# Optimization experiments

Hardware: AMD Instinct MI355X
Metric: run time of the kernel (lower is better)

Reference implementation:

```python
import jax, jax.numpy as jnp
import numpy as np

DIM = 192
WINDOW = 8
HEADS = 6
N = WINDOW * WINDOW


def _relative_position_index(ws):
    coords = np.stack(np.meshgrid(np.arange(ws), np.arange(ws), indexing='ij'))  # (2, ws, ws)
    flat = coords.reshape(2, -1)  # (2, N)
    rel = flat[:, :, None] - flat[:, None, :]  # (2, N, N)
    rel = rel.transpose(1, 2, 0).copy()
    rel[:, :, 0] += ws - 1
    rel[:, :, 1] += ws - 1
    rel[:, :, 0] *= 2 * ws - 1
    return rel.sum(-1).astype(np.int32)  # (N, N)


def setup_inputs() -> dict:
    key = jax.random.key(0)
    ks = jax.random.split(key, 5)
    B_ = 4096
    x = jax.random.normal(ks[0], (B_, N, DIM), dtype=jnp.float32)
    qkv_w = jax.random.normal(ks[1], (3 * DIM, DIM), dtype=jnp.float32) * 0.02
    qkv_b = jnp.zeros((3 * DIM,), dtype=jnp.float32)
    proj_w = jax.random.normal(ks[2], (DIM, DIM), dtype=jnp.float32) * 0.02
    proj_b = jnp.zeros((DIM,), dtype=jnp.float32)
    rpb_table = jax.random.normal(ks[3], ((2 * WINDOW - 1) ** 2, HEADS), dtype=jnp.float32) * 0.02
    rel_idx = jnp.asarray(_relative_position_index(WINDOW))
    return {"x": x, "qkv_w": qkv_w, "qkv_b": qkv_b, "proj_w": proj_w,
            "proj_b": proj_b, "rpb_table": rpb_table, "rel_idx": rel_idx}


def reference(x, qkv_w, qkv_b, proj_w, proj_b, rpb_table, rel_idx):
    B_, n, C = x.shape
    d = C // HEADS
    scale = d ** -0.5
    qkv = x @ qkv_w.T + qkv_b                      # (B_, N, 3C)
    qkv = qkv.reshape(B_, n, 3, HEADS, d).transpose(2, 0, 3, 1, 4)  # (3, B_, H, N, d)
    q, k, v = qkv[0], qkv[1], qkv[2]
    attn = jnp.einsum('bhnd,bhmd->bhnm', q * scale, k)  # (B_, H, N, N)
    bias = rpb_table[rel_idx.reshape(-1)].reshape(n, n, HEADS).transpose(2, 0, 1)  # (H, N, N)
    attn = jax.nn.softmax(attn + bias[None], axis=-1)
    out = jnp.einsum('bhnm,bhmd->bnhd', attn, v).reshape(B_, n, C)
    return out @ proj_w.T + proj_b
```

## Files before the change

### kernel.cpp

```cpp
#include <hip/hip_runtime.h>


constexpr int NT = 64, DIMC = 192, NH = 6;
constexpr float SC = 0.17677669529663687f;

typedef short          s8v __attribute__((ext_vector_type(8)));
typedef float          f4v __attribute__((ext_vector_type(4)));
typedef unsigned short u4v __attribute__((ext_vector_type(4)));

constexpr size_t WS_QKVW  = 0;
constexpr size_t WS_PROJW = WS_QKVW + (size_t)36*6*2*1024;
constexpr size_t WS_BIAS  = WS_PROJW + (size_t)12*6*2*1024;
constexpr size_t WS_QKVB  = WS_BIAS + (size_t)6*4*4*64*16;
constexpr size_t WS_NEED  = WS_QKVB + (size_t)576*4;

__device__ __forceinline__ unsigned short bhi(float x) {
  return (unsigned short)(__builtin_bit_cast(unsigned int, x) >> 16);
}
__device__ __forceinline__ float bft(unsigned short h) {
  return __builtin_bit_cast(float, ((unsigned int)h) << 16);
}
__device__ __forceinline__ unsigned short brne(float x) {
  unsigned int u = __builtin_bit_cast(unsigned int, x);
  u += 0x7FFFu + ((u >> 16) & 1u);
  return (unsigned short)(u >> 16);
}

#define MFMA16(a, b, c) __builtin_amdgcn_mfma_f32_16x16x32_bf16((a), (b), (c), 0, 0, 0)

__device__ __forceinline__ s8v ld_frag(const unsigned short* base, int idx) {
  u4v a = *(const u4v*)(base + idx);
  u4v b = *(const u4v*)(base + idx + 16);
  s8v r;
  #pragma unroll
  for (int i = 0; i < 4; ++i) { r[i] = (short)a[i]; r[4 + i] = (short)b[i]; }
  return r;
}

__global__ __launch_bounds__(256) void prep_kernel(
    const float* __restrict__ qkv_w, const float* __restrict__ qkv_b,
    const float* __restrict__ proj_w, const float* __restrict__ rpb,
    const int* __restrict__ ridx, char* __restrict__ ws)
{
  const int t = blockIdx.x * 256 + threadIdx.x;
  if (t < 13824) {
    const int lane = t & 63, rest = t >> 6;
    const int kk = rest % 6, nt = rest / 6;
    const int g = lane >> 4, c = lane & 15;
    const int n = 16 * nt + c;
    const float sc = (nt < 12) ? SC : 1.f;
    const float* p = qkv_w + n * 192 + kk * 32 + 4 * g;
    f4v a = *(const f4v*)p;       a *= sc;
    f4v b = *(const f4v*)(p + 16); b *= sc;
    s8v hi, lo;
    #pragma unroll
    for (int i = 0; i < 4; ++i) {
      unsigned short h0 = bhi(a[i]); hi[i]     = (short)h0; lo[i]     = (short)brne(a[i] - bft(h0));
      unsigned short h1 = bhi(b[i]); hi[4 + i] = (short)h1; lo[4 + i] = (short)brne(b[i] - bft(h1));
    }
    s8v* base = (s8v*)(ws + WS_QKVW);
    base[((nt * 6 + kk) * 2 + 0) * 64 + lane] = hi;
    base[((nt * 6 + kk) * 2 + 1) * 64 + lane] = lo;
  } else if (t < 18432) {
    const int t2 = t - 13824;
    const int lane = t2 & 63, rest = t2 >> 6;
    const int h = rest % 6, nt = rest / 6;
    const int g = lane >> 4, c = lane & 15;
    const int n = 16 * nt + c;
    const float* p = proj_w + n * 192 + 32 * h + 4 * g;
    f4v a = *(const f4v*)p;
    f4v b = *(const f4v*)(p + 16);
    s8v hi, lo;
    #pragma unroll
    for (int i = 0; i < 4; ++i) {
      unsigned short h0 = bhi(a[i]); hi[i]     = (short)h0; lo[i]     = (short)brne(a[i] - bft(h0));
      unsigned short h1 = bhi(b[i]); hi[4 + i] = (short)h1; lo[4 + i] = (short)brne(b[i] - bft(h1));
    }
    s8v* base = (s8v*)(ws + WS_PROJW);
    base[((nt * 6 + h) * 2 + 0) * 64 + lane] = hi;
    base[((nt * 6 + h) * 2 + 1) * 64 + lane] = lo;
  } else if (t < 24576) {
    const int t2 = t - 18432;
    const int lane = t2 & 63, rest = t2 >> 6;
    const int nt = rest & 3, mt = (rest >> 2) & 3, h = rest >> 4;
    const int g = lane >> 4, c = lane & 15;
    const int q = 16 * nt + c;
    const int kb = 16 * mt + 4 * g;
    const int* ip = ridx + q * 64 + kb;
    f4v o;
    #pragma unroll
    for (int r = 0; r < 4; ++r) o[r] = rpb[ip[r] * 6 + h];
    ((f4v*)(ws + WS_BIAS))[((h * 4 + mt) * 4 + nt) * 64 + lane] = o;
  } else if (t < 25152) {
    const int i = t - 24576;
    ((float*)(ws + WS_QKVB))[i] = qkv_b[i] * (i < 192 ? SC : 1.f);
  }
}


__device__ __forceinline__ void qkv_head(int lane, const float* __restrict__ xbase,
                                         const s8v* __restrict__ qkvw,
                                         int h, f4v acc[6]) {
  #pragma unroll
  for (int j = 0; j < 6; ++j)
    #pragma unroll
    for (int r = 0; r < 4; ++r) acc[j][r] = 0.f;
  #pragma unroll
  for (int kk = 0; kk < 6; ++kk) {
    f4v xa = *(const f4v*)(xbase + 32 * kk);
    f4v xb = *(const f4v*)(xbase + 32 * kk + 16);
    s8v ah, al;
    #pragma unroll
    for (int i = 0; i < 4; ++i) {
      unsigned short h0 = bhi(xa[i]); ah[i]     = (short)h0; al[i]     = (short)brne(xa[i] - bft(h0));
      unsigned short h1 = bhi(xb[i]); ah[4 + i] = (short)h1; al[4 + i] = (short)brne(xb[i] - bft(h1));
    }
    #pragma unroll
    for (int sgj = 0; sgj < 6; ++sgj) {
      const int seg = sgj >> 1, j = sgj & 1;
      const int n576 = seg * 12 + 2 * h + j;
      const s8v bh = qkvw[((n576 * 6 + kk) * 2 + 0) * 64 + lane];
      const s8v bl = qkvw[((n576 * 6 + kk) * 2 + 1) * 64 + lane];
      acc[sgj] = MFMA16(ah, bh, acc[sgj]);
      acc[sgj] = MFMA16(ah, bl, acc[sgj]);
      acc[sgj] = MFMA16(al, bh, acc[sgj]);
    }
  }
}

__device__ __forceinline__ void qkv_stage(int wv, int g, int c,
    const f4v acc[6], const float* __restrict__ qkvb, int h,
    unsigned short* Qh_, unsigned short* Ql_,
    unsigned short* Kh_, unsigned short* Kl_,
    unsigned short* Vh_, unsigned short* Vl_) {
  #pragma unroll
  for (int sgj = 0; sgj < 6; ++sgj) {
    const int seg = sgj >> 1, j = sgj & 1;
    const float bv = qkvb[seg * 192 + 32 * h + 16 * j + c];
    if (seg < 2) {
      unsigned short* dh = (seg == 0) ? Qh_ : Kh_;
      unsigned short* dl = (seg == 0) ? Ql_ : Kl_;
      #pragma unroll
      for (int r = 0; r < 4; ++r) {
        const float v = acc[sgj][r] + bv;
        const unsigned short hh = bhi(v);
        dh[(16 * wv + 4 * g + r) * 36 + 16 * j + c] = hh;
        dl[(16 * wv + 4 * g + r) * 36 + 16 * j + c] = brne(v - bft(hh));
      }
    } else {
      u4v hh, ll;
      #pragma unroll
      for (int r = 0; r < 4; ++r) {
        const float v = acc[sgj][r] + bv;
        const unsigned short x0 = bhi(v);
        hh[r] = x0; ll[r] = brne(v - bft(x0));
      }
      *(u4v*)&Vh_[(16 * j + c) * 68 + 16 * wv + 4 * g] = hh;
      *(u4v*)&Vl_[(16 * j + c) * 68 + 16 * wv + 4 * g] = ll;
    }
  }
}

__device__ __forceinline__ void proj_acc(int lane, const s8v oh, const s8v ol,
                                         const s8v* __restrict__ projw, int h,
                                         f4v pacc[12]) {
  #pragma unroll
  for (int nt = 0; nt < 12; ++nt) {
    const s8v wh = projw[((nt * 6 + h) * 2 + 0) * 64 + lane];
    const s8v wl = projw[((nt * 6 + h) * 2 + 1) * 64 + lane];
    pacc[nt] = MFMA16(oh, wh, pacc[nt]);
    pacc[nt] = MFMA16(oh, wl, pacc[nt]);
    pacc[nt] = MFMA16(ol, wh, pacc[nt]);
  }
}

template<bool DO_NEXT>
__device__ __forceinline__ void head_iter(
    int h, int lane, int wv, int g, int c,
    const float* __restrict__ xbase,
    const s8v* __restrict__ qkvw, const f4v* __restrict__ biasf,
    const float* __restrict__ qkvb,
    const unsigned short* Qhc, const unsigned short* Qlc,
    const unsigned short* Khc, const unsigned short* Klc,
    const unsigned short* Vhc, const unsigned short* Vlc,
    unsigned short* Qhn, unsigned short* Qln,
    unsigned short* Khn, unsigned short* Kln,
    unsigned short* Vhn, unsigned short* Vln,
    s8v& oh, s8v& ol)
{
  f4v sacc[4];
  #pragma unroll
  for (int mt = 0; mt < 4; ++mt)
    sacc[mt] = biasf[((h * 4 + mt) * 4 + wv) * 64 + lane];
  s8v qbh, qbl;
  {
    const int idx = (16 * wv + c) * 36 + 4 * g;
    qbh = ld_frag(Qhc, idx);
    qbl = ld_frag(Qlc, idx);
  }
  #pragma unroll
  for (int mt = 0; mt < 4; ++mt) {
    const int idx = (16 * mt + c) * 36 + 4 * g;
    const s8v kh = ld_frag(Khc, idx);
    const s8v kl = ld_frag(Klc, idx);
    sacc[mt] = MFMA16(kh, qbh, sacc[mt]);
    sacc[mt] = MFMA16(kh, qbl, sacc[mt]);
    sacc[mt] = MFMA16(kl, qbh, sacc[mt]);
  }

  f4v acc2[6];
  if (DO_NEXT) qkv_head(lane, xbase, qkvw, h + 1, acc2);

  float mx = sacc[0][0];
  #pragma unroll
  for (int mt = 0; mt < 4; ++mt)
    #pragma unroll
    for (int r = 0; r < 4; ++r) mx = fmaxf(mx, sacc[mt][r]);
  mx = fmaxf(mx, __shfl_xor(mx, 16));
  mx = fmaxf(mx, __shfl_xor(mx, 32));
  float pv[4][4];
  float sum = 0.f;
  #pragma unroll
  for (int mt = 0; mt < 4; ++mt)
    #pragma unroll
    for (int r = 0; r < 4; ++r) { pv[mt][r] = __expf(sacc[mt][r] - mx); sum += pv[mt][r]; }

  f4v oa0, oa1;
  #pragma unroll
  for (int r = 0; r < 4; ++r) { oa0[r] = 0.f; oa1[r] = 0.f; }
  #pragma unroll
  for (int kk = 0; kk < 2; ++kk) {
    s8v pbh, pbl;
    #pragma unroll
    for (int i = 0; i < 4; ++i) {
      const float v0 = pv[2 * kk][i];
      const float v1 = pv[2 * kk + 1][i];
      const unsigned short h0 = bhi(v0), h1 = bhi(v1);
      pbh[i]     = (short)h0; pbl[i]     = (short)brne(v0 - bft(h0));
      pbh[4 + i] = (short)h1; pbl[4 + i] = (short)brne(v1 - bft(h1));
    }
    #pragma unroll
    for (int mo = 0; mo < 2; ++mo) {
      const int idx = (16 * mo + c) * 68 + 32 * kk + 4 * g;
      const s8v vh = ld_frag(Vhc, idx);
      const s8v vl = ld_frag(Vlc, idx);
      f4v& o = (mo == 0) ? oa0 : oa1;
      o = MFMA16(vh, pbh, o);
      o = MFMA16(vh, pbl, o);
      o = MFMA16(vl, pbh, o);
    }
  }
  sum += __shfl_xor(sum, 16);
  sum += __shfl_xor(sum, 32);
  const float inv = 1.f / sum;

  #pragma unroll
  for (int i = 0; i < 4; ++i) {
    const float v0 = oa0[i] * inv;
    const unsigned short h0 = bhi(v0);
    oh[i] = (short)h0; ol[i] = (short)brne(v0 - bft(h0));
    const float v1 = oa1[i] * inv;
    const unsigned short h1 = bhi(v1);
    oh[4 + i] = (short)h1; ol[4 + i] = (short)brne(v1 - bft(h1));
  }

  if (DO_NEXT) qkv_stage(wv, g, c, acc2, qkvb, h + 1, Qhn, Qln, Khn, Kln, Vhn, Vln);
}

__global__ __launch_bounds__(256, 2)
void win_attn_mfma(const float* __restrict__ x, const float* __restrict__ proj_b,
                   const char* __restrict__ ws, float* __restrict__ out)
{
  __shared__ alignas(16) unsigned short QhS[2][64 * 36], QlS[2][64 * 36];
  __shared__ alignas(16) unsigned short KhS[2][64 * 36], KlS[2][64 * 36];
  __shared__ alignas(16) unsigned short VhS[2][32 * 68], VlS[2][32 * 68];

  const int tid = threadIdx.x;
  const int wv = tid >> 6, lane = tid & 63, g = lane >> 4, c = lane & 15;
  const size_t win = blockIdx.x;
  const float* xw   = x   + win * (size_t)(NT * DIMC);
  float*       outw = out + win * (size_t)(NT * DIMC);

  const s8v*   qkvw  = (const s8v*)(ws + WS_QKVW);
  const s8v*   projw = (const s8v*)(ws + WS_PROJW);
  const f4v*   biasf = (const f4v*)(ws + WS_BIAS);
  const float* qkvb  = (const float*)(ws + WS_QKVB);

  f4v pacc[12];
  #pragma unroll
  for (int i = 0; i < 12; ++i)
    #pragma unroll
    for (int r = 0; r < 4; ++r) pacc[i][r] = 0.f;

  const float* xbase = xw + (size_t)(16 * wv + c) * DIMC + 4 * g;

  {
    f4v acc0[6];
    qkv_head(lane, xbase, qkvw, 0, acc0);
    qkv_stage(wv, g, c, acc0, qkvb, 0,
              QhS[0], QlS[0], KhS[0], KlS[0], VhS[0], VlS[0]);
  }
  __syncthreads();

  s8v oh{}, ol{};

  head_iter<true>(0, lane, wv, g, c, xbase, qkvw, biasf, qkvb,
                  QhS[0], QlS[0], KhS[0], KlS[0], VhS[0], VlS[0],
                  QhS[1], QlS[1], KhS[1], KlS[1], VhS[1], VlS[1],
                  oh, ol);
  __syncthreads();

  #pragma unroll 1
  for (int h = 1; h < NH - 1; ++h) {
    const int p = h & 1;
    proj_acc(lane, oh, ol, projw, h - 1, pacc);
    head_iter<true>(h, lane, wv, g, c, xbase, qkvw, biasf, qkvb,
                    QhS[p], QlS[p], KhS[p], KlS[p], VhS[p], VlS[p],
                    QhS[p ^ 1], QlS[p ^ 1], KhS[p ^ 1], KlS[p ^ 1],
                    VhS[p ^ 1], VlS[p ^ 1],
                    oh, ol);
    __syncthreads();
  }

  proj_acc(lane, oh, ol, projw, 4, pacc);
  head_iter<false>(5, lane, wv, g, c, xbase, qkvw, biasf, qkvb,
                   QhS[1], QlS[1], KhS[1], KlS[1], VhS[1], VlS[1],
                   QhS[0], QlS[0], KhS[0], KlS[0], VhS[0], VlS[0],
                   oh, ol);
  proj_acc(lane, oh, ol, projw, 5, pacc);

  #pragma unroll
  for (int nt = 0; nt < 12; ++nt) {
    const float pb = proj_b[16 * nt + c];
    #pragma unroll
    for (int r = 0; r < 4; ++r)
      outw[(size_t)(16 * wv + 4 * g + r) * DIMC + 16 * nt + c] = pacc[nt][r] + pb;
  }
}

__global__ __launch_bounds__(256, 2)
void win_attn_kernel(const float* __restrict__ x, const float* __restrict__ qkv_w,
                     const float* __restrict__ qkv_b, const float* __restrict__ proj_w,
                     const float* __restrict__ proj_b, const float* __restrict__ rpb,
                     const int* __restrict__ ridx, float* __restrict__ out)
{
  __shared__ float reg1[32 * 192];
  __shared__ float reg2[48 * 64];
  __shared__ float qs[64 * 36];
  __shared__ float ks[64 * 36];
  __shared__ float vs[64 * 36];

  const int tid = threadIdx.x;
  const int w = blockIdx.x;
  const float* xw = x + (size_t)w * (NT * DIMC);
  float* outw = out + (size_t)w * (NT * DIMC);

  const int cg = tid >> 4;
  const int tgA = tid & 15;
  const int tB = tid >> 2;
  const int jB = tid & 3;
  const int ogD = tid >> 4;
  const int tgD = tid & 15;

  int idxv[16];
  #pragma unroll
  for (int mm = 0; mm < 16; ++mm) idxv[mm] = ridx[tB * 64 + jB + 4 * mm] * NH;

  float oacc[4][12];
  #pragma unroll
  for (int tt = 0; tt < 4; ++tt)
    #pragma unroll
    for (int oo = 0; oo < 12; ++oo) oacc[tt][oo] = 0.f;

  for (int h = 0; h < NH; ++h) {
    float acc[6][4];
    #pragma unroll
    for (int cc = 0; cc < 6; ++cc)
      #pragma unroll
      for (int tt = 0; tt < 4; ++tt) acc[cc][tt] = 0.f;

    for (int i0 = 0; i0 < DIMC; i0 += 48) {
      __syncthreads();
      #pragma unroll
      for (int k = 0; k < 12; ++k) {
        int flat = k * 256 + tid;
        int t = flat & 63, ii = flat >> 6;
        reg2[ii * 64 + t] = xw[t * DIMC + i0 + ii];
      }
      #pragma unroll
      for (int k = 0; k < 18; ++k) {
        int flat = k * 256 + tid;
        int rr = flat % 96, ii = flat / 96;
        int seg = rr >> 5, lc = rr & 31;
        int grow = seg * 192 + h * 32 + lc;
        reg1[ii * 96 + rr] = qkv_w[grow * DIMC + i0 + ii];
      }
      __syncthreads();
      #pragma unroll 2
      for (int i = 0; i < 48; ++i) {
        float4 x4 = *(const float4*)(&reg2[i * 64 + 4 * tgA]);
        const float* wr = &reg1[i * 96 + 6 * cg];
        float2 w0 = *(const float2*)(wr + 0);
        float2 w1 = *(const float2*)(wr + 2);
        float2 w2 = *(const float2*)(wr + 4);
        float xa[4] = {x4.x, x4.y, x4.z, x4.w};
        float wa[6] = {w0.x, w0.y, w1.x, w1.y, w2.x, w2.y};
        #pragma unroll
        for (int cc = 0; cc < 6; ++cc)
          #pragma unroll
          for (int tt = 0; tt < 4; ++tt)
            acc[cc][tt] = fmaf(wa[cc], xa[tt], acc[cc][tt]);
      }
    }
    #pragma unroll
    for (int cc = 0; cc < 6; ++cc) {
      int cch = 6 * cg + cc;
      int seg = cch >> 5, lc = cch & 31;
      float bv = qkv_b[seg * 192 + h * 32 + lc];
      if (seg == 0) {
        #pragma unroll
        for (int tt = 0; tt < 4; ++tt)
          qs[(4 * tgA + tt) * 36 + lc] = (acc[cc][tt] + bv) * SC;
      } else if (seg == 1) {
        #pragma unroll
        for (int tt = 0; tt < 4; ++tt)
          ks[(4 * tgA + tt) * 36 + lc] = acc[cc][tt] + bv;
      } else {
        #pragma unroll
        for (int tt = 0; tt < 4; ++tt)
          vs[(4 * tgA + tt) * 36 + lc] = acc[cc][tt] + bv;
      }
    }
    __syncthreads();

    #pragma unroll
    for (int k = 0; k < 24; ++k) {
      int flat = k * 256 + tid;
      int o = flat % 192, ccc = flat / 192;
      reg1[ccc * 192 + o] = proj_w[o * DIMC + h * 32 + ccc];
    }

    float qr[32];
    {
      const float* qrow = &qs[tB * 36];
      #pragma unroll
      for (int d4 = 0; d4 < 8; ++d4) {
        float4 q4 = *(const float4*)(qrow + 4 * d4);
        qr[4*d4+0] = q4.x; qr[4*d4+1] = q4.y; qr[4*d4+2] = q4.z; qr[4*d4+3] = q4.w;
      }
    }
    float sv[16];
    #pragma unroll
    for (int mm = 0; mm < 16; ++mm) {
      const float* krow = &ks[(jB + 4 * mm) * 36];
      float a = rpb[idxv[mm] + h];
      #pragma unroll
      for (int d4 = 0; d4 < 8; ++d4) {
        float4 k4 = *(const float4*)(krow + 4 * d4);
        a = fmaf(qr[4*d4+0], k4.x, a);
        a = fmaf(qr[4*d4+1], k4.y, a);
        a = fmaf(qr[4*d4+2], k4.z, a);
        a = fmaf(qr[4*d4+3], k4.w, a);
      }
      sv[mm] = a;
    }
    float mx = sv[0];
    #pragma unroll
    for (int mm = 1; mm < 16; ++mm) mx = fmaxf(mx, sv[mm]);
    mx = fmaxf(mx, __shfl_xor(mx, 1));
    mx = fmaxf(mx, __shfl_xor(mx, 2));
    float sum = 0.f;
    #pragma unroll
    for (int mm = 0; mm < 16; ++mm) { sv[mm] = __expf(sv[mm] - mx); sum += sv[mm]; }
    sum += __shfl_xor(sum, 1);
    sum += __shfl_xor(sum, 2);
    const float inv = 1.f / sum;

    float part[32];
    #pragma unroll
    for (int dd = 0; dd < 32; ++dd) part[dd] = 0.f;
    #pragma unroll
    for (int mm = 0; mm < 16; ++mm) {
      float pvv = sv[mm] * inv;
      const float* vrow = &vs[(jB + 4 * mm) * 36];
      #pragma unroll
      for (int d4 = 0; d4 < 8; ++d4) {
        float4 v4 = *(const float4*)(vrow + 4 * d4);
        part[4*d4+0] = fmaf(pvv, v4.x, part[4*d4+0]);
        part[4*d4+1] = fmaf(pvv, v4.y, part[4*d4+1]);
        part[4*d4+2] = fmaf(pvv, v4.z, part[4*d4+2]);
        part[4*d4+3] = fmaf(pvv, v4.w, part[4*d4+3]);
      }
    }
    float p16[16];
    {
      const bool hi2 = (jB & 1);
      #pragma unroll
      for (int k2 = 0; k2 < 16; ++k2) {
        float lo_v = part[k2], hi_v = part[16 + k2];
        float sendv = hi2 ? lo_v : hi_v;
        float keepv = hi2 ? hi_v : lo_v;
        float got = __shfl_xor(sendv, 1);
        p16[k2] = keepv + got;
      }
    }
    float p8[8];
    {
      const bool hi2 = (jB & 2);
      #pragma unroll
      for (int k2 = 0; k2 < 8; ++k2) {
        float lo_v = p16[k2], hi_v = p16[8 + k2];
        float sendv = hi2 ? lo_v : hi_v;
        float keepv = hi2 ? hi_v : lo_v;
        float got = __shfl_xor(sendv, 2);
        p8[k2] = keepv + got;
      }
    }
    const int dd0 = (jB & 1) * 16 + (jB & 2) * 4;
    #pragma unroll
    for (int k2 = 0; k2 < 8; ++k2)
      reg2[(dd0 + k2) * 64 + tB] = p8[k2];

    __syncthreads();

    {
      const int o0 = 12 * ogD, t0 = 4 * tgD;
      #pragma unroll 2
      for (int cc2 = 0; cc2 < 32; ++cc2) {
        float4 a4 = *(const float4*)(&reg2[cc2 * 64 + t0]);
        const float* pr = &reg1[cc2 * 192 + o0];
        float4 b0 = *(const float4*)(pr + 0);
        float4 b1 = *(const float4*)(pr + 4);
        float4 b2 = *(const float4*)(pr + 8);
        float av[4]  = {a4.x, a4.y, a4.z, a4.w};
        float bw[12] = {b0.x, b0.y, b0.z, b0.w, b1.x, b1.y, b1.z, b1.w,
                        b2.x, b2.y, b2.z, b2.w};
        #pragma unroll
        for (int tt = 0; tt < 4; ++tt)
          #pragma unroll
          for (int oo = 0; oo < 12; ++oo)
            oacc[tt][oo] = fmaf(av[tt], bw[oo], oacc[tt][oo]);
      }
    }
  }

  {
    const int o0 = 12 * ogD, t0 = 4 * tgD;
    #pragma unroll
    for (int oo = 0; oo < 12; ++oo) {
      float pb = proj_b[o0 + oo];
      #pragma unroll
      for (int tt = 0; tt < 4; ++tt)
        outw[(size_t)(t0 + tt) * DIMC + o0 + oo] = oacc[tt][oo] + pb;
    }
  }
}

extern "C" void kernel_launch(void* const* d_in, const int* in_sizes, int n_in,
                              void* d_out, int out_size, void* d_ws, size_t ws_size,
                              hipStream_t stream) {
  const float* x      = (const float*)d_in[0];
  const float* qkv_w  = (const float*)d_in[1];
  const float* qkv_b  = (const float*)d_in[2];
  const float* proj_w = (const float*)d_in[3];
  const float* proj_b = (const float*)d_in[4];
  const float* rpb    = (const float*)d_in[5];
  const int*   ridx   = (const int*)d_in[6];
  float* out = (float*)d_out;
  const int B = in_sizes[0] / (NT * DIMC);

  if (d_ws != nullptr && ws_size >= WS_NEED) {
    hipLaunchKernelGGL(prep_kernel, dim3(99), dim3(256), 0, stream,
                       qkv_w, qkv_b, proj_w, rpb, ridx, (char*)d_ws);
    hipLaunchKernelGGL(win_attn_mfma, dim3(B), dim3(256), 0, stream,
                       x, proj_b, (const char*)d_ws, out);
  } else {
    hipLaunchKernelGGL(win_attn_kernel, dim3(B), dim3(256), 0, stream,
                       x, qkv_w, qkv_b, proj_w, proj_b, rpb, ridx, out);
  }
}
```

Before: 937.4 us.

## Warp-specialize window attention into QKV producer and attention consumer waves

The block grows from 4 to 6 waves. Two producer waves compute the QKV projection for the next head into a double-buffered LDS area, while four consumer waves run attention, softmax and the output projection for the current head. The two roles hand off through block barriers. The intent is to overlap the QKV GEMM with attention work that the old code ran serially within each wave. The cost is that producer waves recompute x fragments for all four row tiles, and the larger 384-thread block with launch bounds (384,3) changes register pressure and occupancy.

```diff
diff --git a/kernel.cpp b/kernel.cpp
--- a/kernel.cpp
+++ b/kernel.cpp
@@ -97,177 +97,87 @@
   }
 }
 
-
-__device__ __forceinline__ void qkv_head(int lane, const float* __restrict__ xbase,
-                                         const s8v* __restrict__ qkvw,
-                                         int h, f4v acc[6]) {
+__device__ __forceinline__ void produce_qkv(
+    int p, int lane, int g, int c, int hh,
+    const float* __restrict__ xw,
+    const s8v* __restrict__ qkvw, const float* __restrict__ qkvb,
+    unsigned short* Qh_, unsigned short* Ql_,
+    unsigned short* Kh_, unsigned short* Kl_,
+    unsigned short* Vh_, unsigned short* Vl_)
+{
+  f4v acc[3][4];
   #pragma unroll
-  for (int j = 0; j < 6; ++j)
-    #pragma unroll
-    for (int r = 0; r < 4; ++r) acc[j][r] = 0.f;
+  for (int s = 0; s < 3; ++s)
+    #pragma unroll
+    for (int mt = 0; mt < 4; ++mt)
+      #pragma unroll
+      for (int r = 0; r < 4; ++r) acc[s][mt][r] = 0.f;
+
   #pragma unroll
   for (int kk = 0; kk < 6; ++kk) {
-    f4v xa = *(const f4v*)(xbase + 32 * kk);
-    f4v xb = *(const f4v*)(xbase + 32 * kk + 16);
-    s8v ah, al;
-    #pragma unroll
-    for (int i = 0; i < 4; ++i) {
-      unsigned short h0 = bhi(xa[i]); ah[i]     = (short)h0; al[i]     = (short)brne(xa[i] - bft(h0));
-      unsigned short h1 = bhi(xb[i]); ah[4 + i] = (short)h1; al[4 + i] = (short)brne(xb[i] - bft(h1));
-    }
-    #pragma unroll
-    for (int sgj = 0; sgj < 6; ++sgj) {
-      const int seg = sgj >> 1, j = sgj & 1;
-      const int n576 = seg * 12 + 2 * h + j;
-      const s8v bh = qkvw[((n576 * 6 + kk) * 2 + 0) * 64 + lane];
-      const s8v bl = qkvw[((n576 * 6 + kk) * 2 + 1) * 64 + lane];
-      acc[sgj] = MFMA16(ah, bh, acc[sgj]);
-      acc[sgj] = MFMA16(ah, bl, acc[sgj]);
-      acc[sgj] = MFMA16(al, bh, acc[sgj]);
-    }
-  }
-}
-
-__device__ __forceinline__ void qkv_stage(int wv, int g, int c,
-    const f4v acc[6], const float* __restrict__ qkvb, int h,
-    unsigned short* Qh_, unsigned short* Ql_,
-    unsigned short* Kh_, unsigned short* Kl_,
-    unsigned short* Vh_, unsigned short* Vl_) {
+    s8v bh[3], bl[3];
+    #pragma unroll
+    for (int s = 0; s < 3; ++s) {
+      const int sgj = 3 * p + s;
+      const int n576 = (sgj >> 1) * 12 + 2 * hh + (sgj & 1);
+      bh[s] = qkvw[((n576 * 6 + kk) * 2 + 0) * 64 + lane];
+      bl[s] = qkvw[((n576 * 6 + kk) * 2 + 1) * 64 + lane];
+    }
+    #pragma unroll
+    for (int mt = 0; mt < 4; ++mt) {
+      const float* xp = xw + (size_t)(16 * mt + c) * DIMC + 32 * kk + 4 * g;
+      f4v xa = *(const f4v*)xp;
+      f4v xb = *(const f4v*)(xp + 16);
+      s8v ah, al;
+      #pragma unroll
+      for (int i = 0; i < 4; ++i) {
+        unsigned short h0 = bhi(xa[i]); ah[i]     = (short)h0; al[i]     = (short)brne(xa[i] - bft(h0));
+        unsigned short h1 = bhi(xb[i]); ah[4 + i] = (short)h1; al[4 + i] = (short)brne(xb[i] - bft(h1));
+      }
+      #pragma unroll
+      for (int s = 0; s < 3; ++s) {
+        acc[s][mt] = MFMA16(ah, bh[s], acc[s][mt]);
+        acc[s][mt] = MFMA16(ah, bl[s], acc[s][mt]);
+        acc[s][mt] = MFMA16(al, bh[s], acc[s][mt]);
+      }
+    }
+  }
+
   #pragma unroll
-  for (int sgj = 0; sgj < 6; ++sgj) {
+  for (int s = 0; s < 3; ++s) {
+    const int sgj = 3 * p + s;
     const int seg = sgj >> 1, j = sgj & 1;
-    const float bv = qkvb[seg * 192 + 32 * h + 16 * j + c];
+    const float bv = qkvb[seg * 192 + 32 * hh + 16 * j + c];
     if (seg < 2) {
       unsigned short* dh = (seg == 0) ? Qh_ : Kh_;
       unsigned short* dl = (seg == 0) ? Ql_ : Kl_;
       #pragma unroll
-      for (int r = 0; r < 4; ++r) {
-        const float v = acc[sgj][r] + bv;
-        const unsigned short hh = bhi(v);
-        dh[(16 * wv + 4 * g + r) * 36 + 16 * j + c] = hh;
-        dl[(16 * wv + 4 * g + r) * 36 + 16 * j + c] = brne(v - bft(hh));
-      }
+      for (int mt = 0; mt < 4; ++mt)
+        #pragma unroll
+        for (int r = 0; r < 4; ++r) {
+          const float v = acc[s][mt][r] + bv;
+          const unsigned short hh0 = bhi(v);
+          dh[(16 * mt + 4 * g + r) * 36 + 16 * j + c] = hh0;
+          dl[(16 * mt + 4 * g + r) * 36 + 16 * j + c] = brne(v - bft(hh0));
+        }
     } else {
-      u4v hh, ll;
-      #pragma unroll
-      for (int r = 0; r < 4; ++r) {
-        const float v = acc[sgj][r] + bv;
-        const unsigned short x0 = bhi(v);
-        hh[r] = x0; ll[r] = brne(v - bft(x0));
-      }
-      *(u4v*)&Vh_[(16 * j + c) * 68 + 16 * wv + 4 * g] = hh;
-      *(u4v*)&Vl_[(16 * j + c) * 68 + 16 * wv + 4 * g] = ll;
-    }
-  }
-}
-
-__device__ __forceinline__ void proj_acc(int lane, const s8v oh, const s8v ol,
-                                         const s8v* __restrict__ projw, int h,
-                                         f4v pacc[12]) {
-  #pragma unroll
-  for (int nt = 0; nt < 12; ++nt) {
-    const s8v wh = projw[((nt * 6 + h) * 2 + 0) * 64 + lane];
-    const s8v wl = projw[((nt * 6 + h) * 2 + 1) * 64 + lane];
-    pacc[nt] = MFMA16(oh, wh, pacc[nt]);
-    pacc[nt] = MFMA16(oh, wl, pacc[nt]);
-    pacc[nt] = MFMA16(ol, wh, pacc[nt]);
-  }
-}
-
-template<bool DO_NEXT>
-__device__ __forceinline__ void head_iter(
-    int h, int lane, int wv, int g, int c,
-    const float* __restrict__ xbase,
-    const s8v* __restrict__ qkvw, const f4v* __restrict__ biasf,
-    const float* __restrict__ qkvb,
-    const unsigned short* Qhc, const unsigned short* Qlc,
-    const unsigned short* Khc, const unsigned short* Klc,
-    const unsigned short* Vhc, const unsigned short* Vlc,
-    unsigned short* Qhn, unsigned short* Qln,
-    unsigned short* Khn, unsigned short* Kln,
-    unsigned short* Vhn, unsigned short* Vln,
-    s8v& oh, s8v& ol)
-{
-  f4v sacc[4];
-  #pragma unroll
-  for (int mt = 0; mt < 4; ++mt)
-    sacc[mt] = biasf[((h * 4 + mt) * 4 + wv) * 64 + lane];
-  s8v qbh, qbl;
-  {
-    const int idx = (16 * wv + c) * 36 + 4 * g;
-    qbh = ld_frag(Qhc, idx);
-    qbl = ld_frag(Qlc, idx);
-  }
-  #pragma unroll
-  for (int mt = 0; mt < 4; ++mt) {
-    const int idx = (16 * mt + c) * 36 + 4 * g;
-    const s8v kh = ld_frag(Khc, idx);
-    const s8v kl = ld_frag(Klc, idx);
-    sacc[mt] = MFMA16(kh, qbh, sacc[mt]);
-    sacc[mt] = MFMA16(kh, qbl, sacc[mt]);
-    sacc[mt] = MFMA16(kl, qbh, sacc[mt]);
-  }
-
-  f4v acc2[6];
-  if (DO_NEXT) qkv_head(lane, xbase, qkvw, h + 1, acc2);
-
-  float mx = sacc[0][0];
-  #pragma unroll
-  for (int mt = 0; mt < 4; ++mt)
-    #pragma unroll
-    for (int r = 0; r < 4; ++r) mx = fmaxf(mx, sacc[mt][r]);
-  mx = fmaxf(mx, __shfl_xor(mx, 16));
-  mx = fmaxf(mx, __shfl_xor(mx, 32));
-  float pv[4][4];
-  float sum = 0.f;
-  #pragma unroll
-  for (int mt = 0; mt < 4; ++mt)
-    #pragma unroll
-    for (int r = 0; r < 4; ++r) { pv[mt][r] = __expf(sacc[mt][r] - mx); sum += pv[mt][r]; }
-
-  f4v oa0, oa1;
-  #pragma unroll
-  for (int r = 0; r < 4; ++r) { oa0[r] = 0.f; oa1[r] = 0.f; }
-  #pragma unroll
-  for (int kk = 0; kk < 2; ++kk) {
-    s8v pbh, pbl;
-    #pragma unroll
-    for (int i = 0; i < 4; ++i) {
-      const float v0 = pv[2 * kk][i];
-      const float v1 = pv[2 * kk + 1][i];
-      const unsigned short h0 = bhi(v0), h1 = bhi(v1);
-      pbh[i]     = (short)h0; pbl[i]     = (short)brne(v0 - bft(h0));
-      pbh[4 + i] = (short)h1; pbl[4 + i] = (short)brne(v1 - bft(h1));
-    }
-    #pragma unroll
-    for (int mo = 0; mo < 2; ++mo) {
-      const int idx = (16 * mo + c) * 68 + 32 * kk + 4 * g;
-      const s8v vh = ld_frag(Vhc, idx);
-      const s8v vl = ld_frag(Vlc, idx);
-      f4v& o = (mo == 0) ? oa0 : oa1;
-      o = MFMA16(vh, pbh, o);
-      o = MFMA16(vh, pbl, o);
-      o = MFMA16(vl, pbh, o);
-    }
-  }
-  sum += __shfl_xor(sum, 16);
-  sum += __shfl_xor(sum, 32);
-  const float inv = 1.f / sum;
-
-  #pragma unroll
-  for (int i = 0; i < 4; ++i) {
-    const float v0 = oa0[i] * inv;
-    const unsigned short h0 = bhi(v0);
-    oh[i] = (short)h0; ol[i] = (short)brne(v0 - bft(h0));
-    const float v1 = oa1[i] * inv;
-    const unsigned short h1 = bhi(v1);
-    oh[4 + i] = (short)h1; ol[4 + i] = (short)brne(v1 - bft(h1));
-  }
-
-  if (DO_NEXT) qkv_stage(wv, g, c, acc2, qkvb, h + 1, Qhn, Qln, Khn, Kln, Vhn, Vln);
-}
-
-__global__ __launch_bounds__(256, 2)
+      #pragma unroll
+      for (int mt = 0; mt < 4; ++mt) {
+        u4v hh4, ll4;
+        #pragma unroll
+        for (int r = 0; r < 4; ++r) {
+          const float v = acc[s][mt][r] + bv;
+          const unsigned short x0 = bhi(v);
+          hh4[r] = x0; ll4[r] = brne(v - bft(x0));
+        }
+        *(u4v*)&Vh_[(16 * j + c) * 68 + 16 * mt + 4 * g] = hh4;
+        *(u4v*)&Vl_[(16 * j + c) * 68 + 16 * mt + 4 * g] = ll4;
+      }
+    }
+  }
+}
+
+__global__ __launch_bounds__(384, 3)
 void win_attn_mfma(const float* __restrict__ x, const float* __restrict__ proj_b,
                    const char* __restrict__ ws, float* __restrict__ out)
 {
@@ -286,55 +196,131 @@
   const f4v*   biasf = (const f4v*)(ws + WS_BIAS);
   const float* qkvb  = (const float*)(ws + WS_QKVB);
 
-  f4v pacc[12];
-  #pragma unroll
-  for (int i = 0; i < 12; ++i)
-    #pragma unroll
-    for (int r = 0; r < 4; ++r) pacc[i][r] = 0.f;
-
-  const float* xbase = xw + (size_t)(16 * wv + c) * DIMC + 4 * g;
-
-  {
-    f4v acc0[6];
-    qkv_head(lane, xbase, qkvw, 0, acc0);
-    qkv_stage(wv, g, c, acc0, qkvb, 0,
-              QhS[0], QlS[0], KhS[0], KlS[0], VhS[0], VlS[0]);
-  }
-  __syncthreads();
-
-  s8v oh{}, ol{};
-
-  head_iter<true>(0, lane, wv, g, c, xbase, qkvw, biasf, qkvb,
-                  QhS[0], QlS[0], KhS[0], KlS[0], VhS[0], VlS[0],
-                  QhS[1], QlS[1], KhS[1], KlS[1], VhS[1], VlS[1],
-                  oh, ol);
-  __syncthreads();
-
-  #pragma unroll 1
-  for (int h = 1; h < NH - 1; ++h) {
-    const int p = h & 1;
-    proj_acc(lane, oh, ol, projw, h - 1, pacc);
-    head_iter<true>(h, lane, wv, g, c, xbase, qkvw, biasf, qkvb,
-                    QhS[p], QlS[p], KhS[p], KlS[p], VhS[p], VlS[p],
-                    QhS[p ^ 1], QlS[p ^ 1], KhS[p ^ 1], KlS[p ^ 1],
-                    VhS[p ^ 1], VlS[p ^ 1],
-                    oh, ol);
+  if (wv < 4) {
+    f4v pacc[12];
+    #pragma unroll
+    for (int i = 0; i < 12; ++i)
+      #pragma unroll
+      for (int r = 0; r < 4; ++r) pacc[i][r] = 0.f;
+
     __syncthreads();
-  }
-
-  proj_acc(lane, oh, ol, projw, 4, pacc);
-  head_iter<false>(5, lane, wv, g, c, xbase, qkvw, biasf, qkvb,
-                   QhS[1], QlS[1], KhS[1], KlS[1], VhS[1], VlS[1],
-                   QhS[0], QlS[0], KhS[0], KlS[0], VhS[0], VlS[0],
-                   oh, ol);
-  proj_acc(lane, oh, ol, projw, 5, pacc);
-
-  #pragma unroll
-  for (int nt = 0; nt < 12; ++nt) {
-    const float pb = proj_b[16 * nt + c];
-    #pragma unroll
-    for (int r = 0; r < 4; ++r)
-      outw[(size_t)(16 * wv + 4 * g + r) * DIMC + 16 * nt + c] = pacc[nt][r] + pb;
+
+    #pragma unroll 1
+    for (int h = 0; h < NH; ++h) {
+      const int b = h & 1;
+      const unsigned short* Qhc = QhS[b], *Qlc = QlS[b];
+      const unsigned short* Khc = KhS[b], *Klc = KlS[b];
+      const unsigned short* Vhc = VhS[b], *Vlc = VlS[b];
+
+      f4v sacc[4];
+      #pragma unroll
+      for (int mt = 0; mt < 4; ++mt)
+        sacc[mt] = biasf[((h * 4 + mt) * 4 + wv) * 64 + lane];
+      s8v qbh, qbl;
+      {
+        const int idx = (16 * wv + c) * 36 + 4 * g;
+        qbh = ld_frag(Qhc, idx);
+        qbl = ld_frag(Qlc, idx);
+      }
+      #pragma unroll
+      for (int mt = 0; mt < 4; ++mt) {
+        const int idx = (16 * mt + c) * 36 + 4 * g;
+        const s8v kh = ld_frag(Khc, idx);
+        const s8v kl = ld_frag(Klc, idx);
+        sacc[mt] = MFMA16(kh, qbh, sacc[mt]);
+        sacc[mt] = MFMA16(kh, qbl, sacc[mt]);
+        sacc[mt] = MFMA16(kl, qbh, sacc[mt]);
+      }
+
+      float mx = sacc[0][0];
+      #pragma unroll
+      for (int mt = 0; mt < 4; ++mt)
+        #pragma unroll
+        for (int r = 0; r < 4; ++r) mx = fmaxf(mx, sacc[mt][r]);
+      mx = fmaxf(mx, __shfl_xor(mx, 16));
+      mx = fmaxf(mx, __shfl_xor(mx, 32));
+      float pv[4][4];
+      float sum = 0.f;
+      #pragma unroll
+      for (int mt = 0; mt < 4; ++mt)
+        #pragma unroll
+        for (int r = 0; r < 4; ++r) { pv[mt][r] = __expf(sacc[mt][r] - mx); sum += pv[mt][r]; }
+
+      f4v oa0, oa1;
+      #pragma unroll
+      for (int r = 0; r < 4; ++r) { oa0[r] = 0.f; oa1[r] = 0.f; }
+      #pragma unroll
+      for (int kk = 0; kk < 2; ++kk) {
+        s8v pbh, pbl;
+        #pragma unroll
+        for (int i = 0; i < 4; ++i) {
+          const float v0 = pv[2 * kk][i];
+          const float v1 = pv[2 * kk + 1][i];
+          const unsigned short h0 = bhi(v0), h1 = bhi(v1);
+          pbh[i]     = (short)h0; pbl[i]     = (short)brne(v0 - bft(h0));
+          pbh[4 + i] = (short)h1; pbl[4 + i] = (short)brne(v1 - bft(h1));
+        }
+        #pragma unroll
+        for (int mo = 0; mo < 2; ++mo) {
+          const int idx = (16 * mo + c) * 68 + 32 * kk + 4 * g;
+          const s8v vh = ld_frag(Vhc, idx);
+          const s8v vl = ld_frag(Vlc, idx);
+          f4v& o = (mo == 0) ? oa0 : oa1;
+          o = MFMA16(vh, pbh, o);
+          o = MFMA16(vh, pbl, o);
+          o = MFMA16(vl, pbh, o);
+        }
+      }
+      sum += __shfl_xor(sum, 16);
+      sum += __shfl_xor(sum, 32);
+      const float inv = 1.f / sum;
+
+      s8v oh, ol;
+      #pragma unroll
+      for (int i = 0; i < 4; ++i) {
+        const float v0 = oa0[i] * inv;
+        const unsigned short h0 = bhi(v0);
+        oh[i] = (short)h0; ol[i] = (short)brne(v0 - bft(h0));
+        const float v1 = oa1[i] * inv;
+        const unsigned short h1 = bhi(v1);
+        oh[4 + i] = (short)h1; ol[4 + i] = (short)brne(v1 - bft(h1));
+      }
+
+      #pragma unroll
+      for (int nt = 0; nt < 12; ++nt) {
+        const s8v wh = projw[((nt * 6 + h) * 2 + 0) * 64 + lane];
+        const s8v wl = projw[((nt * 6 + h) * 2 + 1) * 64 + lane];
+        pacc[nt] = MFMA16(oh, wh, pacc[nt]);
+        pacc[nt] = MFMA16(oh, wl, pacc[nt]);
+        pacc[nt] = MFMA16(ol, wh, pacc[nt]);
+      }
+
+      __syncthreads();
+    }
+
+    #pragma unroll
+    for (int nt = 0; nt < 12; ++nt) {
+      const float pb = proj_b[16 * nt + c];
+      #pragma unroll
+      for (int r = 0; r < 4; ++r)
+        outw[(size_t)(16 * wv + 4 * g + r) * DIMC + 16 * nt + c] = pacc[nt][r] + pb;
+    }
+  } else {
+    const int p = wv - 4;
+
+    produce_qkv(p, lane, g, c, 0, xw, qkvw, qkvb,
+                QhS[0], QlS[0], KhS[0], KlS[0], VhS[0], VlS[0]);
+    __syncthreads();
+
+    #pragma unroll 1
+    for (int h = 0; h < NH; ++h) {
+      if (h < NH - 1) {
+        const int nb = (h + 1) & 1;
+        produce_qkv(p, lane, g, c, h + 1, xw, qkvw, qkvb,
+                    QhS[nb], QlS[nb], KhS[nb], KlS[nb], VhS[nb], VlS[nb]);
+      }
+      __syncthreads();
+    }
   }
 }
 
@@ -572,7 +558,7 @@
   if (d_ws != nullptr && ws_size >= WS_NEED) {
     hipLaunchKernelGGL(prep_kernel, dim3(99), dim3(256), 0, stream,
                        qkv_w, qkv_b, proj_w, rpb, ridx, (char*)d_ws);
-    hipLaunchKernelGGL(win_attn_mfma, dim3(B), dim3(256), 0, stream,
+    hipLaunchKernelGGL(win_attn_mfma, dim3(B), dim3(384), 0, stream,
                        x, proj_b, (const char*)d_ws, out);
   } else {
     hipLaunchKernelGGL(win_attn_kernel, dim3(B), dim3(256), 0, stream,
```

Result: slower. 1.331 ms (+41.9%).
